# Optimization experiments

Hardware: AMD Instinct MI355X
Metric: run time of the kernel (lower is better)

## Reference

```python
import jax, jax.numpy as jnp
import numpy as np

B, T, NB = 8, 120, 40
VD, WD = 2053, 300
H, E, NH, HD = 512, 256, 8, 64
SEG, NSEG = 12, 10
IDX = np.round(np.linspace(SEG - 1, T - 1, NSEG)).astype(int)  # segment endpoints


def setup_inputs():
    keys = iter(jax.random.split(jax.random.key(0), 64))
    def w(*shape):
        return jax.random.normal(next(keys), shape, jnp.float32) * 0.02
    z = lambda *s: jnp.zeros(s, jnp.float32)
    return dict(
        videos=jax.random.normal(next(keys), (B, T, NB, VD), jnp.float32),
        sub_glove=jax.random.normal(next(keys), (B, WD), jnp.float32),
        obj_glove=jax.random.normal(next(keys), (B, WD), jnp.float32),
        W_ev=w(VD - 5, E), b_ev=z(E),
        W_el=w(5, E), b_el=z(E),
        W_ew=w(WD, E), b_ew=z(E),
        W_sp1=w(2 * E, E), b_sp1=z(E), w_sp2=w(E),
        W_s2o=w(NB, E), b_s2o=z(E),
        W_o2s=w(NB, E), b_o2s=z(E),
        W_tv=w(H, H), b_tv=z(H),
        Wq=w(H, H), bq=z(H), Wk=w(H, H), bk=z(H), Wv=w(H, H), bv=z(H), Wo=w(H, H), bo=z(H),
        g1=jnp.ones(H, jnp.float32), be1=z(H),
        Wf1=w(H, H), bf1=z(H), Wf2=w(H, H), bf2=z(H),
        g2=jnp.ones(H, jnp.float32), be2=z(H),
        W_tr=w(H, H), b_tr=z(H),
        W_tb1=w(2 * H, H), b_tb1=z(H), w_tb2=w(H),
        W_ih=w(4 * H, H), W_hh=w(4 * H, H), b_ih=z(4 * H), b_hh=z(4 * H),
        W_l1=w(2 * H, H), b_l1=z(H), w_l2=w(H),
    )


def reference(videos, sub_glove, obj_glove, W_ev, b_ev, W_el, b_el, W_ew, b_ew,
              W_sp1, b_sp1, w_sp2, W_s2o, b_s2o, W_o2s, b_o2s, W_tv, b_tv,
              Wq, bq, Wk, bk, Wv, bv, Wo, bo, g1, be1, Wf1, bf1, Wf2, bf2, g2, be2,
              W_tr, b_tr, W_tb1, b_tb1, w_tb2, W_ih, W_hh, b_ih, b_hh, W_l1, b_l1, w_l2):
    relu = jax.nn.relu
    # spatialAtt (vectorized over batch; dropout = identity, eval mode)
    ve = relu(videos[..., :VD - 5] @ W_ev + b_ev) + relu(videos[..., VD - 5:] @ W_el + b_el)  # [B,T,NB,E]
    sub_e = relu(sub_glove @ W_ew + b_ew)  # [B,E]
    obj_e = relu(obj_glove @ W_ew + b_ew)

    def attend(word):  # additive attention over bboxes per frame
        wb = jnp.broadcast_to(word[:, None, None, :], ve.shape)
        s = jnp.tanh(jnp.concatenate([ve, wb], -1) @ W_sp1 + b_sp1) @ w_sp2  # [B,T,NB]
        a = jax.nn.softmax(s, -1)
        return jnp.einsum('btn,btne->bte', a, ve), a

    sub_feat, sub_att = attend(sub_e)
    obj_feat, obj_att = attend(obj_e)
    s2o = relu(sub_att @ W_s2o + b_s2o)  # msg_sub2obj on attention weights [B,T,NB]->[B,T,E]
    o2s = relu(obj_att @ W_o2s + b_o2s)
    ori_x = jnp.concatenate([sub_feat + o2s, obj_feat + s2o], -1)  # [B,T,H]
    rel = jnp.concatenate([sub_e, obj_e], -1)[:, None, :]  # [B,1,H]

    def ln(zz, g, b):
        m = zz.mean(-1, keepdims=True)
        v = jnp.mean((zz - m) ** 2, -1, keepdims=True)
        return (zz - m) * jax.lax.rsqrt(v + 1e-5) * g + b

    # transform_visual + 1-layer post-norm TransformerEncoder (relu FFN, dropout=identity)
    x = relu(ori_x @ W_tv + b_tv)
    q = (x @ Wq + bq).reshape(B, T, NH, HD)
    k = (x @ Wk + bk).reshape(B, T, NH, HD)
    v = (x @ Wv + bv).reshape(B, T, NH, HD)
    att = jax.nn.softmax(jnp.einsum('bqhd,bkhd->bhqk', q, k) / np.float32(np.sqrt(HD)), -1)
    ao = jnp.einsum('bhqk,bkhd->bqhd', att, v).reshape(B, T, H) @ Wo + bo
    x = ln(x + ao, g1, be1)
    x = ln(x + relu(x @ Wf1 + bf1) @ Wf2 + bf2, g2, be2)
    within = x  # [B,T,H]

    seg_in = within[:, IDX, :]  # [B,NSEG,H]
    tr = relu(rel @ W_tr + b_tr)
    ctx = jnp.broadcast_to(tr, seg_in.shape)
    beta2 = jax.nn.softmax(jnp.tanh(jnp.concatenate([seg_in, ctx], -1) @ W_tb1 + b_tb1) @ w_tb2, -1)  # [B,NSEG]

    # torch-convention LSTM (gates i,f,g,o); note attention weights are NOT applied to input (vfeat=input)
    def step(carry, xt):
        h, c = carry
        gates = xt @ W_ih.T + h @ W_hh.T + b_ih + b_hh
        i, f, g_, o = jnp.split(gates, 4, -1)
        c = jax.nn.sigmoid(f) * c + jax.nn.sigmoid(i) * jnp.tanh(g_)
        h = jax.nn.sigmoid(o) * jnp.tanh(c)
        return (h, c), h

    (hT, cT), _ = jax.lax.scan(step, (jnp.zeros((B, H), within.dtype), jnp.zeros((B, H), within.dtype)),
                               seg_in.transpose(1, 0, 2))

    ctx2 = jnp.broadcast_to(hT[:, None, :], within.shape)
    beta1 = jax.nn.softmax(jnp.tanh(jnp.concatenate([within, ctx2], -1) @ W_l1 + b_l1) @ w_l2, -1)  # [B,T]
    temp = beta1 + jnp.repeat(beta2, SEG, axis=1)  # temp[:,i] = beta1[:,i] + beta2[:,i//12]
    output = jnp.einsum('bt,bth->bh', temp, within)  # [B,H]
    return output, hT, cT, sub_att, obj_att, beta1, beta2
```

## Files before the change

kernel.cpp:

```cpp
#include <hip/hip_runtime.h>
#include <cstddef>
#include <cstdint>

#define B_ 8
#define T_ 120
#define NB_ 40
#define VD_ 2053
#define E_ 256
#define H_ 512
#define M_ 38400
#define R_ 960

static constexpr size_t OFF_VE    = 0;
static constexpr size_t OFF_SSUB  = OFF_VE + (size_t)M_ * E_;
static constexpr size_t OFF_SOBJ  = OFF_SSUB + M_;
static constexpr size_t OFF_WBS   = OFF_SOBJ + M_;
static constexpr size_t OFF_WBO   = OFF_WBS + B_ * E_;
static constexpr size_t OFF_TBIAS = OFF_WBO + B_ * E_;
static constexpr size_t OFF_ORIX  = OFF_TBIAS + B_ * H_;
static constexpr size_t OFF_X     = OFF_ORIX + (size_t)R_ * H_;
static constexpr size_t OFF_Q     = OFF_X    + (size_t)R_ * H_;
static constexpr size_t OFF_K     = OFF_Q    + (size_t)R_ * H_;
static constexpr size_t OFF_V     = OFF_K    + (size_t)R_ * H_;
static constexpr size_t OFF_AO    = OFF_V    + (size_t)R_ * H_;
static constexpr size_t OFF_ATTN  = OFF_AO   + (size_t)R_ * H_;
static constexpr size_t OFF_X1    = OFF_ATTN + (size_t)R_ * H_;
static constexpr size_t OFF_F1    = OFF_X1   + (size_t)R_ * H_;
static constexpr size_t OFF_F2    = OFF_F1   + (size_t)R_ * H_;
static constexpr size_t OFF_WIN   = OFF_F2   + (size_t)R_ * H_;
static constexpr size_t OFF_WT    = OFF_WIN  + (size_t)R_ * H_;
static constexpr size_t OFF_Z2    = OFF_WT + (size_t)1024 * 2048;
static constexpr size_t OFF_H0    = OFF_Z2 + 128;
static constexpr size_t OFF_HB    = OFF_H0 + 3 * 4096;
static constexpr size_t OFF_L1    = OFF_HB + B_ * H_;
static constexpr size_t OFF_BAR   = OFF_L1 + 960;
static constexpr size_t OFF_END0  = OFF_BAR + 4;
static constexpr size_t OFF_WIH   = (OFF_END0 + 3) & ~(size_t)3;
static constexpr size_t OFF_WHH   = OFF_WIH + 524288;
static constexpr size_t OFF_WL1B  = OFF_WHH + 524288;
static constexpr size_t OFF_WINBF = OFF_WL1B + 131072;
static constexpr size_t OFF_VEBF  = OFF_WINBF + 245760;
static constexpr size_t OFF_END   = OFF_VEBF + (size_t)M_ * E_ / 2;

static constexpr size_t O_OUT  = 0;
static constexpr size_t O_HT   = 4096;
static constexpr size_t O_CT   = 8192;
static constexpr size_t O_SATT = 12288;
static constexpr size_t O_OATT = 50688;
static constexpr size_t O_B1   = 89088;
static constexpr size_t O_B2   = 90048;

#define DEVFN __device__ __forceinline__

typedef __attribute__((ext_vector_type(8))) short short8;
typedef __attribute__((ext_vector_type(4))) float f32x4;

DEVFN float sigf(float x) { return 1.0f / (1.0f + __expf(-x)); }

DEVFN float fast_tanh(float x) {
  float e = __expf(2.f * x);
  return 1.f - 2.f / (e + 1.f);
}

DEVFN unsigned short f2bf(float x) {
  unsigned int u = __float_as_uint(x);
  u += 0x7FFFu + ((u >> 16) & 1u);
  return (unsigned short)(u >> 16);
}
DEVFN float bf2f(unsigned short u) { return __uint_as_float((unsigned int)u << 16); }

DEVFN short8 mk8(const float* f) {
  short8 r;
#pragma unroll
  for (int j = 0; j < 8; ++j) r[j] = (short)f2bf(f[j]);
  return r;
}

DEVFN float wredsum(float v) {
#pragma unroll
  for (int m = 32; m; m >>= 1) v += __shfl_xor(v, m);
  return v;
}
DEVFN float wredmax(float v) {
#pragma unroll
  for (int m = 32; m; m >>= 1) v = fmaxf(v, __shfl_xor(v, m));
  return v;
}

__global__ __launch_bounds__(256) void k_zero(float* p, int n) {
  int i = blockIdx.x * 256 + threadIdx.x;
  if (i < n) p[i] = 0.f;
}

__global__ __launch_bounds__(256) void k_small0(
    const float* __restrict__ sub_g, const float* __restrict__ obj_g,
    const float* __restrict__ W_ew, const float* __restrict__ b_ew,
    const float* __restrict__ W_sp1, const float* __restrict__ b_sp1,
    const float* __restrict__ W_tr, const float* __restrict__ b_tr,
    const float* __restrict__ W_tb1, const float* __restrict__ b_tb1,
    float* __restrict__ wbs, float* __restrict__ wbo, float* __restrict__ tbias) {
  int b = blockIdx.x, tid = threadIdx.x;
  __shared__ float sg[300], og[300], se[256], oe[256], trl[512];
  for (int i = tid; i < 300; i += 256) { sg[i] = sub_g[b * 300 + i]; og[i] = obj_g[b * 300 + i]; }
  __syncthreads();
  {
    float a1 = b_ew[tid], a2 = a1;
    for (int w = 0; w < 300; ++w) {
      float we = W_ew[w * 256 + tid];
      a1 += sg[w] * we; a2 += og[w] * we;
    }
    se[tid] = fmaxf(a1, 0.f); oe[tid] = fmaxf(a2, 0.f);
  }
  __syncthreads();
  {
    float a1 = b_sp1[tid], a2 = a1;
    for (int e = 0; e < 256; ++e) {
      float ww = W_sp1[(256 + e) * 256 + tid];
      a1 += se[e] * ww; a2 += oe[e] * ww;
    }
    wbs[b * 256 + tid] = a1; wbo[b * 256 + tid] = a2;
  }
  for (int jj = 0; jj < 2; ++jj) {
    int j = tid + jj * 256;
    float a = b_tr[j];
    for (int i = 0; i < 256; ++i) a += se[i] * W_tr[i * 512 + j];
    for (int i = 0; i < 256; ++i) a += oe[i] * W_tr[(256 + i) * 512 + j];
    trl[j] = fmaxf(a, 0.f);
  }
  __syncthreads();
  for (int jj = 0; jj < 2; ++jj) {
    int j = tid + jj * 256;
    float a = b_tb1[j];
    for (int i = 0; i < 512; ++i) a += trl[i] * W_tb1[(size_t)(512 + i) * 512 + j];
    tbias[b * 512 + j] = a;
  }
}

__global__ __launch_bounds__(256) void k_wprep(
    const float* __restrict__ W_ev, const float* __restrict__ W_tv,
    const float* __restrict__ Wq, const float* __restrict__ Wk,
    const float* __restrict__ Wv, const float* __restrict__ Wo,
    const float* __restrict__ Wf1, const float* __restrict__ Wf2,
    const float* __restrict__ W_sp1, const float* __restrict__ W_l1,
    const float* __restrict__ W_ih, const float* __restrict__ W_hh,
    const float* __restrict__ sub_g, const float* __restrict__ obj_g,
    const float* __restrict__ W_ew, const float* __restrict__ b_ew,
    const float* __restrict__ b_sp1, const float* __restrict__ W_tr,
    const float* __restrict__ b_tr, const float* __restrict__ W_tb1,
    const float* __restrict__ b_tb1,
    unsigned short* __restrict__ wevbf, unsigned short* __restrict__ w7bf,
    unsigned short* __restrict__ wsp1bf, unsigned short* __restrict__ wl1bf,
    unsigned short* __restrict__ wihbf, unsigned short* __restrict__ whhbf,
    float* __restrict__ hz,
    float* __restrict__ wbs, float* __restrict__ wbo, float* __restrict__ tbias) {
  int bid = blockIdx.x, tid = threadIdx.x;
  __shared__ float shm[64 * 65];
  float (*t)[65] = (float(*)[65])shm;
  if (bid < 128) {
    int kb = bid >> 2, nb = bid & 3;
#pragma unroll
    for (int i = 0; i < 16; ++i) {
      int idx = tid + 256 * i; int r = idx >> 6, c = idx & 63;
      t[r][c] = W_ev[(size_t)(kb * 64 + r) * 256 + nb * 64 + c];
    }
    __syncthreads();
#pragma unroll
    for (int i = 0; i < 16; ++i) {
      int idx = tid + 256 * i; int n = idx >> 6, kk = idx & 63;
      wevbf[(size_t)(nb * 64 + n) * 2048 + kb * 64 + kk] = f2bf(t[kk][n]);
    }
  } else if (bid < 576) {
    int b2 = bid - 128;
    int wsel = b2 >> 6, sub = b2 & 63;
    int kb = sub >> 3, nb = sub & 7;
    const float* src = wsel == 0 ? W_tv : wsel == 1 ? Wq : wsel == 2 ? Wk
                     : wsel == 3 ? Wv : wsel == 4 ? Wo : wsel == 5 ? Wf1 : Wf2;
    unsigned short* dst = w7bf + (size_t)wsel * 262144;
#pragma unroll
    for (int i = 0; i < 16; ++i) {
      int idx = tid + 256 * i; int r = idx >> 6, c = idx & 63;
      t[r][c] = src[(size_t)(kb * 64 + r) * 512 + nb * 64 + c];
    }
    __syncthreads();
#pragma unroll
    for (int i = 0; i < 16; ++i) {
      int idx = tid + 256 * i; int n = idx >> 6, kk = idx & 63;
      dst[(size_t)(nb * 64 + n) * 512 + kb * 64 + kk] = f2bf(t[kk][n]);
    }
  } else if (bid < 592) {
    int b2 = bid - 576;
    int kb = b2 >> 2, nb = b2 & 3;
#pragma unroll
    for (int i = 0; i < 16; ++i) {
      int idx = tid + 256 * i; int r = idx >> 6, c = idx & 63;
      t[r][c] = W_sp1[(size_t)(kb * 64 + r) * 256 + nb * 64 + c];
    }
    __syncthreads();
#pragma unroll
    for (int i = 0; i < 16; ++i) {
      int idx = tid + 256 * i; int n = idx >> 6, kk = idx & 63;
      wsp1bf[(size_t)(nb * 64 + n) * 256 + kb * 64 + kk] = f2bf(t[kk][n]);
    }
  } else if (bid < 656) {
    int b2 = bid - 592;
    int kb = b2 >> 3, nb = b2 & 7;
#pragma unroll
    for (int i = 0; i < 16; ++i) {
      int idx = tid + 256 * i; int r = idx >> 6, c = idx & 63;
      t[r][c] = W_l1[(size_t)(kb * 64 + r) * 512 + nb * 64 + c];
    }
    __syncthreads();
#pragma unroll
    for (int i = 0; i < 16; ++i) {
      int idx = tid + 256 * i; int n = idx >> 6, kk = idx & 63;
      wl1bf[(size_t)(nb * 64 + n) * 512 + kb * 64 + kk] = f2bf(t[kk][n]);
    }
  } else if (bid < 1680) {
    int i = (bid - 656) * 256 + tid;
    const float* s; unsigned short* d; int off;
    if (i < 131072) { s = W_ih; d = wihbf; off = i * 8; }
    else            { s = W_hh; d = whhbf; off = (i - 131072) * 8; }
    float f[8];
#pragma unroll
    for (int j = 0; j < 8; ++j) f[j] = s[off + j];
    *(short8*)(d + off) = mk8(f);
  } else if (bid == 1680) {
    for (int i = tid; i < 12288; i += 256) hz[i] = 0.f;
  } else {
    int b = bid - 1681;
    float* sg = shm;
    float* og = shm + 300;
    float* se = shm + 600;
    float* oe = shm + 856;
    float* trl = shm + 1112;
    for (int i = tid; i < 300; i += 256) { sg[i] = sub_g[b * 300 + i]; og[i] = obj_g[b * 300 + i]; }
    __syncthreads();
    {
      float a1 = b_ew[tid], a2 = a1;
      for (int w = 0; w < 300; ++w) {
        float we = W_ew[w * 256 + tid];
        a1 += sg[w] * we; a2 += og[w] * we;
      }
      se[tid] = fmaxf(a1, 0.f); oe[tid] = fmaxf(a2, 0.f);
    }
    __syncthreads();
    {
      float a1 = b_sp1[tid], a2 = a1;
      for (int e = 0; e < 256; ++e) {
        float ww = W_sp1[(256 + e) * 256 + tid];
        a1 += se[e] * ww; a2 += oe[e] * ww;
      }
      wbs[b * 256 + tid] = a1; wbo[b * 256 + tid] = a2;
    }
    for (int jj = 0; jj < 2; ++jj) {
      int j = tid + jj * 256;
      float a = b_tr[j];
      for (int i = 0; i < 256; ++i) a += se[i] * W_tr[i * 512 + j];
      for (int i = 0; i < 256; ++i) a += oe[i] * W_tr[(256 + i) * 512 + j];
      trl[j] = fmaxf(a, 0.f);
    }
    __syncthreads();
    for (int jj = 0; jj < 2; ++jj) {
      int j = tid + jj * 256;
      float a = b_tb1[j];
      for (int i = 0; i < 512; ++i) a += trl[i] * W_tb1[(size_t)(512 + i) * 512 + j];
      tbias[b * 512 + j] = a;
    }
  }
}

__global__ __launch_bounds__(256) void k_wconvT(const float* __restrict__ src,
                                                unsigned short* __restrict__ dst,
                                                int K, int N) {
  __shared__ float t[64][65];
  int nblk = N >> 6;
  int kb = blockIdx.x / nblk, nb = blockIdx.x - kb * nblk;
  int tid = threadIdx.x;
#pragma unroll
  for (int i = 0; i < 16; ++i) {
    int idx = tid + 256 * i;
    int r = idx >> 6, c = idx & 63;
    t[r][c] = src[(size_t)(kb * 64 + r) * N + nb * 64 + c];
  }
  __syncthreads();
#pragma unroll
  for (int i = 0; i < 16; ++i) {
    int idx = tid + 256 * i;
    int n = idx >> 6, kk = idx & 63;
    dst[(size_t)(nb * 64 + n) * K + kb * 64 + kk] = f2bf(t[kk][n]);
  }
}

__global__ __launch_bounds__(256) void k_wconv7(
    const float* __restrict__ w0, const float* __restrict__ w1,
    const float* __restrict__ w2, const float* __restrict__ w3,
    const float* __restrict__ w4, const float* __restrict__ w5,
    const float* __restrict__ w6, unsigned short* __restrict__ dstb) {
  __shared__ float t[64][65];
  int wsel = blockIdx.x >> 6, sub = blockIdx.x & 63;
  int kb = sub >> 3, nb = sub & 7;
  const float* src = wsel == 0 ? w0 : wsel == 1 ? w1 : wsel == 2 ? w2
                   : wsel == 3 ? w3 : wsel == 4 ? w4 : wsel == 5 ? w5 : w6;
  unsigned short* dst = dstb + (size_t)wsel * 262144;
  int tid = threadIdx.x;
#pragma unroll
  for (int i = 0; i < 16; ++i) {
    int idx = tid + 256 * i;
    int r = idx >> 6, c = idx & 63;
    t[r][c] = src[(size_t)(kb * 64 + r) * 512 + nb * 64 + c];
  }
  __syncthreads();
#pragma unroll
  for (int i = 0; i < 16; ++i) {
    int idx = tid + 256 * i;
    int n = idx >> 6, kk = idx & 63;
    dst[(size_t)(nb * 64 + n) * 512 + kb * 64 + kk] = f2bf(t[kk][n]);
  }
}

__global__ __launch_bounds__(256) void k_cvt2(const float* __restrict__ a,
                                              const float* __restrict__ b,
                                              unsigned short* __restrict__ da,
                                              unsigned short* __restrict__ db) {
  int i = blockIdx.x * 256 + threadIdx.x;
  const float* s; unsigned short* d; int off;
  if (i < 131072) { s = a; d = da; off = i * 8; }
  else            { s = b; d = db; off = (i - 131072) * 8; }
  float f[8];
#pragma unroll
  for (int j = 0; j < 8; ++j) f[j] = s[off + j];
  *(short8*)(d + off) = mk8(f);
}

#define VESTEP(FA, KA, KB)                                                 \
  {                                                                        \
    short8 ha = mk8(FA);                                                   \
    __syncthreads();                                                       \
    *(short8*)(lds + dstA) = ha;                                           \
    _Pragma("unroll")                                                      \
    for (int i = 0; i < 4; ++i) *(short8*)(lds + dstB[i]) = stB[i];        \
    __syncthreads();                                                       \
    _Pragma("unroll")                                                      \
    for (int j = 0; j < 8; ++j) FA[j] = apA[(KA) + j];                     \
    _Pragma("unroll")                                                      \
    for (int i = 0; i < 4; ++i) stB[i] = *(const short8*)(spB[i] + (KB));  \
    _Pragma("unroll")                                                      \
    for (int kk = 0; kk < 2; ++kk) {                                       \
      short8 a8[4], b8[2];                                                 \
      _Pragma("unroll")                                                    \
      for (int fm = 0; fm < 4; ++fm) {                                     \
        int row = fm * 16 + l16;                                           \
        a8[fm] = *(const short8*)(lds + row * 64 +                         \
                                  (((kk * 4 + lk) ^ (row & 7)) * 8));      \
      }                                                                    \
      _Pragma("unroll")                                                    \
      for (int fn = 0; fn < 2; ++fn) {                                     \
        int n = wid * 32 + fn * 16 + l16;                                  \
        b8[fn] = *(const short8*)(lds + 4096 + n * 64 +                    \
                                  (((kk * 4 + lk) ^ (n & 7)) * 8));        \
      }                                                                    \
      _Pragma("unroll")                                                    \
      for (int fm = 0; fm < 4; ++fm)                                       \
        _Pragma("unroll")                                                  \
        for (int fn = 0; fn < 2; ++fn)                                     \
          acc[fm][fn] = __builtin_amdgcn_mfma_f32_16x16x32_bf16(           \
              a8[fm], b8[fn], acc[fm][fn], 0, 0, 0);                       \
    }                                                                      \
  }

__global__ __launch_bounds__(512) void k_gemm_ve_m97(
    const float* __restrict__ videos, const unsigned short* __restrict__ wtbf,
    const float* __restrict__ bev, const float* __restrict__ Wel,
    const float* __restrict__ bel, unsigned short* __restrict__ vebf) {
  __shared__ __align__(16) unsigned short lds[20480];
  int tid = threadIdx.x;
  int rowbase = blockIdx.x * 64;
  int lane = tid & 63, wid = tid >> 6;
  int l16 = lane & 15, lk = lane >> 4;

  int arow = tid >> 3, akc = tid & 7;
  const float* apA = videos + (size_t)(rowbase + arow) * VD_ + akc * 8;
  int dstA = arow * 64 + ((akc ^ (arow & 7)) * 8);
  const unsigned short* spB[4];
  int dstB[4];
#pragma unroll
  for (int i = 0; i < 4; ++i) {
    int g = tid + 512 * i;
    int n = g >> 3, kc = g & 7;
    spB[i] = wtbf + (size_t)n * 2048 + kc * 8;
    dstB[i] = 4096 + n * 64 + ((kc ^ (n & 7)) * 8);
  }
  float fa0[8], fa1[8];
  short8 stB[4];
#pragma unroll
  for (int j = 0; j < 8; ++j) fa0[j] = apA[j];
#pragma unroll
  for (int i = 0; i < 4; ++i) stB[i] = *(const short8*)(spB[i]);
#pragma unroll
  for (int j = 0; j < 8; ++j) fa1[j] = apA[64 + j];

  f32x4 acc[4][2] = {};
  for (int k0 = 0; k0 < 2048; k0 += 128) {
    int ka0 = k0 + 128; if (ka0 >= 2048) ka0 -= 2048;
    int kb0 = k0 + 64;
    VESTEP(fa0, ka0, kb0);
    int ka1 = k0 + 192; if (ka1 >= 2048) ka1 -= 2048;
    int kb1 = k0 + 128; if (kb1 >= 2048) kb1 -= 2048;
    VESTEP(fa1, ka1, kb1);
  }
  float bevv[2], belv[2], w5[5][2];
#pragma unroll
  for (int fn = 0; fn < 2; ++fn) {
    int col = wid * 32 + fn * 16 + l16;
    bevv[fn] = bev[col]; belv[fn] = bel[col];
#pragma unroll
    for (int kk = 0; kk < 5; ++kk) w5[kk][fn] = Wel[kk * 256 + col];
  }
#pragma unroll
  for (int fm = 0; fm < 4; ++fm) {
#pragma unroll
    for (int r = 0; r < 4; ++r) {
      int grow = rowbase + fm * 16 + lk * 4 + r;
      const float* vt = videos + (size_t)grow * VD_ + 2048;
      float t0 = vt[0], t1 = vt[1], t2 = vt[2], t3 = vt[3], t4 = vt[4];
      unsigned short* vob = vebf + (size_t)grow * 256;
#pragma unroll
      for (int fn = 0; fn < 2; ++fn) {
        int col = wid * 32 + fn * 16 + l16;
        float s2 = belv[fn] + t0 * w5[0][fn] + t1 * w5[1][fn] + t2 * w5[2][fn] +
                   t3 * w5[3][fn] + t4 * w5[4][fn];
        float vvv = fmaxf(acc[fm][fn][r] + bevv[fn], 0.f) + fmaxf(s2, 0.f);
        vob[col] = f2bf(vvv);
      }
    }
  }
}

__global__ __launch_bounds__(256) void k_score_bf(
    const unsigned short* __restrict__ vebf, const unsigned short* __restrict__ wsp1,
    const float* __restrict__ w_sp2, const float* __restrict__ wbs,
    const float* __restrict__ wbo, float* __restrict__ s_sub,
    float* __restrict__ s_obj) {
  __shared__ float reds[4][64], redo_[4][64];
  int tid = threadIdx.x;
  int rowbase = blockIdx.x * 64;
  int lane = tid & 63, wid = tid >> 6;
  int l16 = lane & 15, lk = lane >> 4;
  const unsigned short* ap[4];
  const unsigned short* bp[4];
#pragma unroll
  for (int fm = 0; fm < 4; ++fm)
    ap[fm] = vebf + (size_t)(rowbase + fm * 16 + l16) * 256 + lk * 8;
#pragma unroll
  for (int fn = 0; fn < 4; ++fn)
    bp[fn] = wsp1 + (size_t)(wid * 64 + fn * 16 + l16) * 256 + lk * 8;
  f32x4 acc[4][4] = {};
#pragma unroll 2
  for (int k0 = 0; k0 < 256; k0 += 32) {
    short8 a8[4], b8[4];
#pragma unroll
    for (int fm = 0; fm < 4; ++fm) a8[fm] = *(const short8*)(ap[fm] + k0);
#pragma unroll
    for (int fn = 0; fn < 4; ++fn) b8[fn] = *(const short8*)(bp[fn] + k0);
#pragma unroll
    for (int fm = 0; fm < 4; ++fm)
#pragma unroll
      for (int fn = 0; fn < 4; ++fn)
        acc[fm][fn] = __builtin_amdgcn_mfma_f32_16x16x32_bf16(
            a8[fm], b8[fn], acc[fm][fn], 0, 0, 0);
  }
  int b = rowbase / 4800;
  float w2[4], bs[4], bo[4];
#pragma unroll
  for (int fn = 0; fn < 4; ++fn) {
    int col = wid * 64 + fn * 16 + l16;
    w2[fn] = w_sp2[col];
    bs[fn] = wbs[b * 256 + col];
    bo[fn] = wbo[b * 256 + col];
  }
  float ps[4][4], po[4][4];
#pragma unroll
  for (int fm = 0; fm < 4; ++fm)
#pragma unroll
    for (int r = 0; r < 4; ++r) {
      float aps = 0, apo = 0;
#pragma unroll
      for (int fn = 0; fn < 4; ++fn) {
        float t = acc[fm][fn][r];
        aps += fast_tanh(t + bs[fn]) * w2[fn];
        apo += fast_tanh(t + bo[fn]) * w2[fn];
      }
      ps[fm][r] = aps;
      po[fm][r] = apo;
    }
#pragma unroll
  for (int m = 1; m < 16; m <<= 1) {
#pragma unroll
    for (int fm = 0; fm < 4; ++fm)
#pragma unroll
      for (int r = 0; r < 4; ++r) {
        ps[fm][r] += __shfl_xor(ps[fm][r], m);
        po[fm][r] += __shfl_xor(po[fm][r], m);
      }
  }
  if (l16 == 0) {
#pragma unroll
    for (int fm = 0; fm < 4; ++fm)
#pragma unroll
      for (int r = 0; r < 4; ++r) {
        int row = fm * 16 + lk * 4 + r;
        reds[wid][row] = ps[fm][r];
        redo_[wid][row] = po[fm][r];
      }
  }
  __syncthreads();
  if (tid < 64) {
    float s1 = reds[0][tid] + reds[1][tid] + reds[2][tid] + reds[3][tid];
    float s2 = redo_[0][tid] + redo_[1][tid] + redo_[2][tid] + redo_[3][tid];
    s_sub[rowbase + tid] = s1;
    s_obj[rowbase + tid] = s2;
  }
}

__global__ __launch_bounds__(256) void k_attend_bf(
    const float* __restrict__ s_sub, const float* __restrict__ s_obj,
    const unsigned short* __restrict__ vebf, const float* __restrict__ W_s2o,
    const float* __restrict__ b_s2o, const float* __restrict__ W_o2s,
    const float* __restrict__ b_o2s, float* __restrict__ out_satt,
    float* __restrict__ out_oatt, float* __restrict__ orix) {
  int row = blockIdx.x;
  int tid = threadIdx.x;
  __shared__ float alds[2][40];
  int wv = tid >> 6, lane = tid & 63;
  if (wv < 2) {
    const float* sarr = (wv ? s_obj : s_sub) + row * 40;
    float v = (lane < 40) ? sarr[lane] : -1e30f;
    float mx = wredmax(v);
    float e = (lane < 40) ? __expf(v - mx) : 0.f;
    float sm = wredsum(e);
    float p = e / sm;
    if (lane < 40) {
      alds[wv][lane] = p;
      (wv ? out_oatt : out_satt)[row * 40 + lane] = p;
    }
  }
  __syncthreads();
  int e = tid;
  const unsigned short* vrow = vebf + (size_t)row * 40 * 256;
  float sf = 0, of = 0, s2o = b_s2o[e], o2s = b_o2s[e];
  for (int n = 0; n < 40; ++n) {
    float as = alds[0][n], aob = alds[1][n];
    float vv = bf2f(vrow[n * 256 + e]);
    sf += as * vv;
    of += aob * vv;
    s2o += as * W_s2o[n * 256 + e];
    o2s += aob * W_o2s[n * 256 + e];
  }
  s2o = fmaxf(s2o, 0.f);
  o2s = fmaxf(o2s, 0.f);
  orix[(size_t)row * 512 + e] = sf + o2s;
  orix[(size_t)row * 512 + 256 + e] = of + s2o;
}

__global__ __launch_bounds__(256) void k_gemm_ve_mfma(
    const float* __restrict__ videos, const unsigned short* __restrict__ wtbf,
    const float* __restrict__ bev, const float* __restrict__ Wel,
    const float* __restrict__ bel, float* __restrict__ ve) {
  int tid = threadIdx.x;
  int rowbase = blockIdx.x * 64;
  int lane = tid & 63, wid = tid >> 6;
  int l16 = lane & 15, lk = lane >> 4;
  const float* ap[4];
  const unsigned short* bp[4];
#pragma unroll
  for (int fm = 0; fm < 4; ++fm)
    ap[fm] = videos + (size_t)(rowbase + fm * 16 + l16) * VD_ + lk * 8;
#pragma unroll
  for (int fn = 0; fn < 4; ++fn)
    bp[fn] = wtbf + (size_t)(wid * 64 + fn * 16 + l16) * 2048 + lk * 8;
  f32x4 acc[4][4] = {};
  for (int k0 = 0; k0 < 2048; k0 += 64) {
#pragma unroll
    for (int kk = 0; kk < 2; ++kk) {
      int ko = k0 + kk * 32;
      short8 a8[4], b8[4];
#pragma unroll
      for (int fm = 0; fm < 4; ++fm) {
        const float* a = ap[fm] + ko;
        float f[8];
#pragma unroll
        for (int j = 0; j < 8; ++j) f[j] = a[j];
        a8[fm] = mk8(f);
      }
#pragma unroll
      for (int fn = 0; fn < 4; ++fn) b8[fn] = *(const short8*)(bp[fn] + ko);
#pragma unroll
      for (int fm = 0; fm < 4; ++fm)
#pragma unroll
        for (int fn = 0; fn < 4; ++fn)
          acc[fm][fn] = __builtin_amdgcn_mfma_f32_16x16x32_bf16(
              a8[fm], b8[fn], acc[fm][fn], 0, 0, 0);
    }
    if ((k0 & 255) == 192) __builtin_amdgcn_s_barrier();
  }
  float bevv[4], belv[4], w5[5][4];
#pragma unroll
  for (int fn = 0; fn < 4; ++fn) {
    int col = wid * 64 + fn * 16 + l16;
    bevv[fn] = bev[col]; belv[fn] = bel[col];
#pragma unroll
    for (int kk = 0; kk < 5; ++kk) w5[kk][fn] = Wel[kk * 256 + col];
  }
#pragma unroll
  for (int fm = 0; fm < 4; ++fm) {
#pragma unroll
    for (int r = 0; r < 4; ++r) {
      int grow = rowbase + fm * 16 + lk * 4 + r;
      const float* vt = videos + (size_t)grow * VD_ + 2048;
      float t0 = vt[0], t1 = vt[1], t2 = vt[2], t3 = vt[3], t4 = vt[4];
      float* vo = ve + (size_t)grow * 256;
#pragma unroll
      for (int fn = 0; fn < 4; ++fn) {
        int col = wid * 64 + fn * 16 + l16;
        float s2 = belv[fn] + t0 * w5[0][fn] + t1 * w5[1][fn] + t2 * w5[2][fn] +
                   t3 * w5[3][fn] + t4 * w5[4][fn];
        vo[col] = fmaxf(acc[fm][fn][r] + bevv[fn], 0.f) + fmaxf(s2, 0.f);
      }
    }
  }
}

__global__ __launch_bounds__(256) void k_score(
    const float* __restrict__ ve, const float* __restrict__ W_sp1,
    const float* __restrict__ w_sp2, const float* __restrict__ wbs,
    const float* __restrict__ wbo, float* __restrict__ s_sub,
    float* __restrict__ s_obj) {
  __shared__ float vel[32][264];
  int tid = threadIdx.x;
  int rowbase = blockIdx.x * 32;
  for (int i = tid; i < 2048; i += 256) {
    int r = i >> 6, c = (i & 63) << 2;
    *(float4*)&vel[r][c] = *(const float4*)&ve[(size_t)(rowbase + r) * 256 + c];
  }
  __syncthreads();
  int wv = tid >> 6, lane = tid & 63;
  int r0 = wv * 8;
  float acc[8][4] = {};
  for (int k = 0; k < 256; ++k) {
    float w4[4];
#pragma unroll
    for (int c = 0; c < 4; ++c) w4[c] = W_sp1[(size_t)k * 256 + c * 64 + lane];
#pragma unroll
    for (int m = 0; m < 8; ++m) {
      float a = vel[r0 + m][k];
#pragma unroll
      for (int c = 0; c < 4; ++c) acc[m][c] += a * w4[c];
    }
  }
  int b = rowbase / 4800;
  float w2[4], bs[4], bo[4];
#pragma unroll
  for (int c = 0; c < 4; ++c) {
    int col = c * 64 + lane;
    w2[c] = w_sp2[col];
    bs[c] = wbs[b * 256 + col];
    bo[c] = wbo[b * 256 + col];
  }
#pragma unroll
  for (int m = 0; m < 8; ++m) {
    float ps = 0, po = 0;
#pragma unroll
    for (int c = 0; c < 4; ++c) {
      float t = acc[m][c];
      ps += fast_tanh(t + bs[c]) * w2[c];
      po += fast_tanh(t + bo[c]) * w2[c];
    }
    ps = wredsum(ps);
    po = wredsum(po);
    if (lane == 0) {
      s_sub[rowbase + r0 + m] = ps;
      s_obj[rowbase + r0 + m] = po;
    }
  }
}

__global__ __launch_bounds__(256) void k_attend(
    const float* __restrict__ s_sub, const float* __restrict__ s_obj,
    const float* __restrict__ ve, const float* __restrict__ W_s2o,
    const float* __restrict__ b_s2o, const float* __restrict__ W_o2s,
    const float* __restrict__ b_o2s, float* __restrict__ out_satt,
    float* __restrict__ out_oatt, float* __restrict__ orix) {
  int row = blockIdx.x;
  int tid = threadIdx.x;
  __shared__ float alds[2][40];
  int wv = tid >> 6, lane = tid & 63;
  if (wv < 2) {
    const float* sarr = (wv ? s_obj : s_sub) + row * 40;
    float v = (lane < 40) ? sarr[lane] : -1e30f;
    float mx = wredmax(v);
    float e = (lane < 40) ? __expf(v - mx) : 0.f;
    float sm = wredsum(e);
    float p = e / sm;
    if (lane < 40) {
      alds[wv][lane] = p;
      (wv ? out_oatt : out_satt)[row * 40 + lane] = p;
    }
  }
  __syncthreads();
  int e = tid;
  const float* vrow = ve + (size_t)row * 40 * 256;
  float sf = 0, of = 0, s2o = b_s2o[e], o2s = b_o2s[e];
  for (int n = 0; n < 40; ++n) {
    float as = alds[0][n], aob = alds[1][n];
    float vv = vrow[n * 256 + e];
// ... 501 lines not shown
}

__global__ __launch_bounds__(256) void k_final(
    const float* __restrict__ l1, const float* __restrict__ z2,
    const float* __restrict__ within, const float* __restrict__ hT,
    const float* __restrict__ cT, float* __restrict__ dout) {
  int b = blockIdx.x;
  int tid = threadIdx.x;
  __shared__ float temp[120];
  __shared__ float b2[10];
  int wv = tid >> 6, lane = tid & 63;
  if (wv == 1) {
    float v = (lane < 10) ? z2[b * 10 + lane] : -1e30f;
    float mx = wredmax(v);
    float e = (lane < 10) ? __expf(v - mx) : 0.f;
    float sm = wredsum(e);
    if (lane < 10) {
      float p = e / sm;
      b2[lane] = p;
      dout[O_B2 + b * 10 + lane] = p;
    }
  }
  if (wv == 0) {
    float v1 = l1[b * 120 + lane];
    float v2 = (lane + 64 < 120) ? l1[b * 120 + 64 + lane] : -1e30f;
    float mx = wredmax(fmaxf(v1, v2));
    float e1 = __expf(v1 - mx);
    float e2 = (lane + 64 < 120) ? __expf(v2 - mx) : 0.f;
    float sm = wredsum(e1 + e2);
    float p1 = e1 / sm;
    dout[O_B1 + b * 120 + lane] = p1;
    temp[lane] = p1;
    if (lane + 64 < 120) {
      float p2 = e2 / sm;
      dout[O_B1 + b * 120 + 64 + lane] = p2;
      temp[64 + lane] = p2;
    }
  }
  __syncthreads();
  for (int t = tid; t < 120; t += 256) temp[t] += b2[t / 12];
  __syncthreads();
  for (int hh = tid; hh < 512; hh += 256) {
    float o = 0;
    for (int t = 0; t < 120; ++t) o += temp[t] * within[(size_t)(b * 120 + t) * 512 + hh];
    dout[O_OUT + b * 512 + hh] = o;
    dout[O_HT + b * 512 + hh] = hT[b * 512 + hh];
    dout[O_CT + b * 512 + hh] = cT[b * 512 + hh];
  }
}

extern "C" void kernel_launch(void* const* d_in, const int* in_sizes, int n_in,
                              void* d_out, int out_size, void* d_ws, size_t ws_size,
                              hipStream_t stream) {
  const float* videos = (const float*)d_in[0];
  const float* sub_g  = (const float*)d_in[1];
  const float* obj_g  = (const float*)d_in[2];
  const float* W_ev   = (const float*)d_in[3];
  const float* b_ev   = (const float*)d_in[4];
  const float* W_el   = (const float*)d_in[5];
  const float* b_el   = (const float*)d_in[6];
  const float* W_ew   = (const float*)d_in[7];
  const float* b_ew   = (const float*)d_in[8];
  const float* W_sp1  = (const float*)d_in[9];
  const float* b_sp1  = (const float*)d_in[10];
  const float* w_sp2  = (const float*)d_in[11];
  const float* W_s2o  = (const float*)d_in[12];
  const float* b_s2o  = (const float*)d_in[13];
  const float* W_o2s  = (const float*)d_in[14];
  const float* b_o2s  = (const float*)d_in[15];
  const float* W_tv   = (const float*)d_in[16];
  const float* b_tv   = (const float*)d_in[17];
  const float* Wq     = (const float*)d_in[18];
  const float* bq     = (const float*)d_in[19];
  const float* Wk     = (const float*)d_in[20];
  const float* bk     = (const float*)d_in[21];
  const float* Wv     = (const float*)d_in[22];
  const float* bv     = (const float*)d_in[23];
  const float* Wo     = (const float*)d_in[24];
  const float* bo     = (const float*)d_in[25];
  const float* g1     = (const float*)d_in[26];
  const float* be1    = (const float*)d_in[27];
  const float* Wf1    = (const float*)d_in[28];
  const float* bf1    = (const float*)d_in[29];
  const float* Wf2    = (const float*)d_in[30];
  const float* bf2    = (const float*)d_in[31];
  const float* g2     = (const float*)d_in[32];
  const float* be2    = (const float*)d_in[33];
  const float* W_tr   = (const float*)d_in[34];
  const float* b_tr   = (const float*)d_in[35];
  const float* W_tb1  = (const float*)d_in[36];
  const float* b_tb1  = (const float*)d_in[37];
  const float* w_tb2  = (const float*)d_in[38];
  const float* W_ih   = (const float*)d_in[39];
  const float* W_hh   = (const float*)d_in[40];
  const float* b_ih   = (const float*)d_in[41];
  const float* b_hh   = (const float*)d_in[42];
  const float* W_l1   = (const float*)d_in[43];
  const float* b_l1   = (const float*)d_in[44];
  const float* w_l2   = (const float*)d_in[45];

  float* out = (float*)d_out;
  float* w = (float*)d_ws;

  float* ve_p   = w + OFF_VE;
  float* ssub_p = w + OFF_SSUB;
  float* sobj_p = w + OFF_SOBJ;
  float* wbs_p  = w + OFF_WBS;
  float* wbo_p  = w + OFF_WBO;
  float* tb_p   = w + OFF_TBIAS;
  float* orix_p = w + OFF_ORIX;
  float* x_p    = w + OFF_X;
  float* q_p    = w + OFF_Q;
  float* k_p    = w + OFF_K;
  float* v_p    = w + OFF_V;
  float* ao_p   = w + OFF_AO;
  float* attn_p = w + OFF_ATTN;
  float* x1_p   = w + OFF_X1;
  float* f1_p   = w + OFF_F1;
  float* f2_p   = w + OFF_F2;
  float* win_p  = w + OFF_WIN;
  float* z2_p   = w + OFF_Z2;
  float* h_p    = w + OFF_H0;
  float* c_p    = h_p + 2 * 4096;
  float* hb_p   = w + OFF_HB;
  float* l1_p   = w + OFF_L1;

  unsigned short* wtbase = (unsigned short*)(w + OFF_WT);
  unsigned short* wevbf = wtbase;
  unsigned short* w7bf  = wtbase + 524288;
  unsigned short* wtvbf = w7bf;
  unsigned short* wqbf  = w7bf + 1 * 262144;
  unsigned short* wobf  = w7bf + 4 * 262144;
  unsigned short* wf1bf = w7bf + 5 * 262144;
  unsigned short* wf2bf = w7bf + 6 * 262144;
  unsigned short* wsp1bf = w7bf + 7 * 262144;
  unsigned short* wihbf  = (unsigned short*)(w + OFF_WIH);
  unsigned short* whhbf  = (unsigned short*)(w + OFF_WHH);
  unsigned short* wl1bf  = (unsigned short*)(w + OFF_WL1B);
  unsigned short* winbf_p = (unsigned short*)(w + OFF_WINBF);
  unsigned short* vebf_p = (unsigned short*)(w + OFF_VEBF);
  float* gx_p = w + OFF_Q;
  const bool big = ws_size >= (size_t)OFF_END * 4;

  if (big) {
    k_wprep<<<1689, 256, 0, stream>>>(W_ev, W_tv, Wq, Wk, Wv, Wo, Wf1, Wf2,
                                      W_sp1, W_l1, W_ih, W_hh, sub_g, obj_g,
                                      W_ew, b_ew, b_sp1, W_tr, b_tr, W_tb1,
                                      b_tb1, wevbf, w7bf, wsp1bf, wl1bf, wihbf,
                                      whhbf, h_p, wbs_p, wbo_p, tb_p);
    k_gemm_ve_m97<<<600, 512, 0, stream>>>(videos, wevbf, b_ev, W_el, b_el,
                                           vebf_p);
    k_score_bf<<<600, 256, 0, stream>>>(vebf_p, wsp1bf, w_sp2, wbs_p, wbo_p,
                                        ssub_p, sobj_p);
    k_attend_bf<<<960, 256, 0, stream>>>(ssub_p, sobj_p, vebf_p, W_s2o, b_s2o,
                                         W_o2s, b_o2s, out + O_SATT,
                                         out + O_OATT, orix_p);
    k_gemm_h<<<240, 256, 0, stream>>>(orix_p, wtvbf, b_tv, b_tv, b_tv, x_p, 8, 1);
    k_gemm_h<<<720, 256, 0, stream>>>(x_p, wqbf, bq, bk, bv, q_p, 24, 0);
    k_mha<<<256, 256, 0, stream>>>(q_p, k_p, v_p, ao_p);
    k_gemm_h<<<240, 256, 0, stream>>>(ao_p, wobf, bo, bo, bo, attn_p, 8, 0);
    k_ln<<<240, 256, 0, stream>>>(x_p, attn_p, g1, be1, x1_p, nullptr);
    k_gemm_h<<<240, 256, 0, stream>>>(x1_p, wf1bf, bf1, bf1, bf1, f1_p, 8, 1);
    k_gemm_h<<<240, 256, 0, stream>>>(f1_p, wf2bf, bf2, bf2, bf2, f2_p, 8, 0);
    k_ln<<<240, 256, 0, stream>>>(x1_p, f2_p, g2, be2, win_p, winbf_p);
    k_xb<<<144, 256, 0, stream>>>(win_p, wihbf, b_ih, b_hh, gx_p, W_tb1, w_tb2,
                                  tb_p, z2_p);
    for (int s = 0; s < 10; ++s) {
      float* hin = h_p + (s & 1) * 4096;
      float* hout = h_p + ((s & 1) ^ 1) * 4096;
      k_lstm_step<<<32, 128, 0, stream>>>(hin, whhbf, gx_p, s, hout, c_p);
    }
    k_hbias<<<16, 256, 0, stream>>>(h_p, W_l1, b_l1, hb_p);
    k_beta1_bf<<<15, 256, 0, stream>>>(winbf_p, wl1bf, w_l2, hb_p, l1_p);
    k_final<<<8, 256, 0, stream>>>(l1_p, z2_p, win_p, h_p, c_p, out);
  } else {
    unsigned short* wihbf_a = (unsigned short*)(w + OFF_Q + 163840);
    unsigned short* whhbf_a = (unsigned short*)(w + OFF_Q + 688128);
    k_zero<<<48, 256, 0, stream>>>(h_p, 3 * 4096);
    k_small0<<<8, 256, 0, stream>>>(sub_g, obj_g, W_ew, b_ew, W_sp1, b_sp1,
                                    W_tr, b_tr, W_tb1, b_tb1, wbs_p, wbo_p, tb_p);
    k_wconvT<<<128, 256, 0, stream>>>(W_ev, wevbf, 2048, 256);
    k_wconv7<<<448, 256, 0, stream>>>(W_tv, Wq, Wk, Wv, Wo, Wf1, Wf2, w7bf);
    k_gemm_ve_mfma<<<600, 256, 0, stream>>>(videos, wevbf, b_ev, W_el, b_el, ve_p);
    k_score<<<1200, 256, 0, stream>>>(ve_p, W_sp1, w_sp2, wbs_p, wbo_p, ssub_p, sobj_p);
    k_attend<<<960, 256, 0, stream>>>(ssub_p, sobj_p, ve_p, W_s2o, b_s2o, W_o2s,
                                      b_o2s, out + O_SATT, out + O_OATT, orix_p);
    k_gemm_h<<<240, 256, 0, stream>>>(orix_p, wtvbf, b_tv, b_tv, b_tv, x_p, 8, 1);
    k_gemm_h<<<720, 256, 0, stream>>>(x_p, wqbf, bq, bk, bv, q_p, 24, 0);
    k_mha<<<256, 256, 0, stream>>>(q_p, k_p, v_p, ao_p);
    k_gemm_h<<<240, 256, 0, stream>>>(ao_p, wobf, bo, bo, bo, attn_p, 8, 0);
    k_ln<<<240, 256, 0, stream>>>(x_p, attn_p, g1, be1, x1_p, nullptr);
    k_gemm_h<<<240, 256, 0, stream>>>(x1_p, wf1bf, bf1, bf1, bf1, f1_p, 8, 1);
    k_gemm_h<<<240, 256, 0, stream>>>(f1_p, wf2bf, bf2, bf2, bf2, f2_p, 8, 0);
    k_ln<<<240, 256, 0, stream>>>(x1_p, f2_p, g2, be2, win_p, nullptr);
    k_cvt2<<<1024, 256, 0, stream>>>(W_ih, W_hh, wihbf_a, whhbf_a);
    k_xproj<<<64, 256, 0, stream>>>(win_p, wihbf_a, b_ih, b_hh, gx_p);
    k_beta2<<<80, 256, 0, stream>>>(win_p, W_tb1, w_tb2, tb_p, z2_p);
    for (int s = 0; s < 10; ++s) {
      float* hin = h_p + (s & 1) * 4096;
      float* hout = h_p + ((s & 1) ^ 1) * 4096;
      k_lstm_step<<<32, 128, 0, stream>>>(hin, whhbf_a, gx_p, s, hout, c_p);
    }
    k_hbias<<<16, 256, 0, stream>>>(h_p, W_l1, b_l1, hb_p);
    k_beta1<<<240, 256, 0, stream>>>(win_p, W_l1, w_l2, hb_p, l1_p);
    k_final<<<8, 256, 0, stream>>>(l1_p, z2_p, win_p, h_p, c_p, out);
  }
}
```

Measured before the change: 631.0 us.

## Double-buffer LDS in video GEMM and vectorize attend kernel per-wave rows

The main video-embedding GEMM moves from a single LDS buffer with two barriers per k-step to a ping-pong double buffer. The next tile's global loads are issued before the MFMA compute, and only one barrier is needed per step, so load latency overlaps compute. The cost is double the LDS footprint, which may lower occupancy. Separately, the attend kernel now processes four rows per block, one wave each, using 4-wide vector loads and stores instead of one row per block with scalar accesses.

Measured after the change: 638.3 us. No clear change (+1.2%).

```diff
diff --git a/kernel.cpp b/kernel.cpp
--- a/kernel.cpp
+++ b/kernel.cpp
@@ -53,6 +53,7 @@
 #define DEVFN __device__ __forceinline__
 
 typedef __attribute__((ext_vector_type(8))) short short8;
+typedef __attribute__((ext_vector_type(4))) short short4v;
 typedef __attribute__((ext_vector_type(4))) float f32x4;
 
 DEVFN float sigf(float x) { return 1.0f / (1.0f + __expf(-x)); }
@@ -332,47 +333,55 @@
   *(short8*)(d + off) = mk8(f);
 }
 
-#define VESTEP(FA, KA, KB)                                                 \
-  {                                                                        \
-    short8 ha = mk8(FA);                                                   \
-    __syncthreads();                                                       \
-    *(short8*)(lds + dstA) = ha;                                           \
-    _Pragma("unroll")                                                      \
-    for (int i = 0; i < 4; ++i) *(short8*)(lds + dstB[i]) = stB[i];        \
-    __syncthreads();                                                       \
-    _Pragma("unroll")                                                      \
-    for (int j = 0; j < 8; ++j) FA[j] = apA[(KA) + j];                     \
-    _Pragma("unroll")                                                      \
-    for (int i = 0; i < 4; ++i) stB[i] = *(const short8*)(spB[i] + (KB));  \
-    _Pragma("unroll")                                                      \
-    for (int kk = 0; kk < 2; ++kk) {                                       \
-      short8 a8[4], b8[2];                                                 \
-      _Pragma("unroll")                                                    \
-      for (int fm = 0; fm < 4; ++fm) {                                     \
-        int row = fm * 16 + l16;                                           \
-        a8[fm] = *(const short8*)(lds + row * 64 +                         \
-                                  (((kk * 4 + lk) ^ (row & 7)) * 8));      \
-      }                                                                    \
-      _Pragma("unroll")                                                    \
-      for (int fn = 0; fn < 2; ++fn) {                                     \
-        int n = wid * 32 + fn * 16 + l16;                                  \
-        b8[fn] = *(const short8*)(lds + 4096 + n * 64 +                    \
-                                  (((kk * 4 + lk) ^ (n & 7)) * 8));        \
-      }                                                                    \
-      _Pragma("unroll")                                                    \
-      for (int fm = 0; fm < 4; ++fm)                                       \
-        _Pragma("unroll")                                                  \
-        for (int fn = 0; fn < 2; ++fn)                                     \
-          acc[fm][fn] = __builtin_amdgcn_mfma_f32_16x16x32_bf16(           \
-              a8[fm], b8[fn], acc[fm][fn], 0, 0, 0);                       \
-    }                                                                      \
+#define VECOMPUTE(RDBASE)                                                   \
+  _Pragma("unroll")                                                         \
+  for (int kk = 0; kk < 2; ++kk) {                                          \
+    short8 a8[4], b8[2];                                                    \
+    _Pragma("unroll")                                                       \
+    for (int fm = 0; fm < 4; ++fm) {                                        \
+      int row = fm * 16 + l16;                                              \
+      a8[fm] = *(const short8*)(lds + (RDBASE) + row * 64 +                 \
+                                (((kk * 4 + lk) ^ (row & 7)) * 8));         \
+    }                                                                       \
+    _Pragma("unroll")                                                       \
+    for (int fn = 0; fn < 2; ++fn) {                                        \
+      int n = wid * 32 + fn * 16 + l16;                                     \
+      b8[fn] = *(const short8*)(lds + (RDBASE) + 4096 + n * 64 +            \
+                                (((kk * 4 + lk) ^ (n & 7)) * 8));           \
+    }                                                                       \
+    _Pragma("unroll")                                                       \
+    for (int fm = 0; fm < 4; ++fm)                                          \
+      _Pragma("unroll")                                                     \
+      for (int fn = 0; fn < 2; ++fn)                                        \
+        acc[fm][fn] = __builtin_amdgcn_mfma_f32_16x16x32_bf16(              \
+            a8[fm], b8[fn], acc[fm][fn], 0, 0, 0);                          \
+  }
+
+#define VESTEP(RDBASE, WRBASE, KNEXT)                                       \
+  {                                                                         \
+    bool pre = (KNEXT) < 2048;                                              \
+    if (pre) {                                                              \
+      _Pragma("unroll")                                                     \
+      for (int j = 0; j < 8; ++j) fa[j] = apA[(KNEXT) + j];                 \
+      _Pragma("unroll")                                                     \
+      for (int i = 0; i < 4; ++i) stB[i] = *(const short8*)(spB[i] + (KNEXT)); \
+    }                                                                       \
+    VECOMPUTE(RDBASE);                                                      \
+    if (pre) {                                                              \
+      short8 ha = mk8(fa);                                                  \
+      *(short8*)(lds + (WRBASE) + dstA) = ha;                               \
+      _Pragma("unroll")                                                     \
+      for (int i = 0; i < 4; ++i)                                           \
+        *(short8*)(lds + (WRBASE) + dstB[i]) = stB[i];                      \
+      __syncthreads();                                                      \
+    }                                                                       \
   }
 
 __global__ __launch_bounds__(512) void k_gemm_ve_m97(
     const float* __restrict__ videos, const unsigned short* __restrict__ wtbf,
     const float* __restrict__ bev, const float* __restrict__ Wel,
     const float* __restrict__ bel, unsigned short* __restrict__ vebf) {
-  __shared__ __align__(16) unsigned short lds[20480];
+  __shared__ __align__(16) unsigned short lds[40960];
   int tid = threadIdx.x;
   int rowbase = blockIdx.x * 64;
   int lane = tid & 63, wid = tid >> 6;
@@ -390,23 +399,24 @@
     spB[i] = wtbf + (size_t)n * 2048 + kc * 8;
     dstB[i] = 4096 + n * 64 + ((kc ^ (n & 7)) * 8);
   }
-  float fa0[8], fa1[8];
+  float fa[8];
   short8 stB[4];
 #pragma unroll
-  for (int j = 0; j < 8; ++j) fa0[j] = apA[j];
+  for (int j = 0; j < 8; ++j) fa[j] = apA[j];
 #pragma unroll
   for (int i = 0; i < 4; ++i) stB[i] = *(const short8*)(spB[i]);
-#pragma unroll
-  for (int j = 0; j < 8; ++j) fa1[j] = apA[64 + j];
+  {
+    short8 ha = mk8(fa);
+    *(short8*)(lds + dstA) = ha;
+#pragma unroll
+    for (int i = 0; i < 4; ++i) *(short8*)(lds + dstB[i]) = stB[i];
+  }
+  __syncthreads();
 
   f32x4 acc[4][2] = {};
   for (int k0 = 0; k0 < 2048; k0 += 128) {
-    int ka0 = k0 + 128; if (ka0 >= 2048) ka0 -= 2048;
-    int kb0 = k0 + 64;
-    VESTEP(fa0, ka0, kb0);
-    int ka1 = k0 + 192; if (ka1 >= 2048) ka1 -= 2048;
-    int kb1 = k0 + 128; if (kb1 >= 2048) kb1 -= 2048;
-    VESTEP(fa1, ka1, kb1);
+    VESTEP(0, 20480, k0 + 64);
+    VESTEP(20480, 0, k0 + 128);
   }
   float bevv[2], belv[2], w5[5][2];
 #pragma unroll
@@ -528,38 +538,60 @@
     const float* __restrict__ b_s2o, const float* __restrict__ W_o2s,
     const float* __restrict__ b_o2s, float* __restrict__ out_satt,
     float* __restrict__ out_oatt, float* __restrict__ orix) {
-  int row = blockIdx.x;
-  int tid = threadIdx.x;
-  __shared__ float alds[2][40];
+  __shared__ float alds[4][2][40];
+  int tid = threadIdx.x;
   int wv = tid >> 6, lane = tid & 63;
-  if (wv < 2) {
-    const float* sarr = (wv ? s_obj : s_sub) + row * 40;
+  int row = blockIdx.x * 4 + wv;
+  {
+    const float* sarr = s_sub + row * 40;
     float v = (lane < 40) ? sarr[lane] : -1e30f;
     float mx = wredmax(v);
     float e = (lane < 40) ? __expf(v - mx) : 0.f;
     float sm = wredsum(e);
-    float p = e / sm;
     if (lane < 40) {
-      alds[wv][lane] = p;
-      (wv ? out_oatt : out_satt)[row * 40 + lane] = p;
-    }
-  }
-  __syncthreads();
-  int e = tid;
-  const unsigned short* vrow = vebf + (size_t)row * 40 * 256;
-  float sf = 0, of = 0, s2o = b_s2o[e], o2s = b_o2s[e];
+      float p = e / sm;
+      alds[wv][0][lane] = p;
+      out_satt[row * 40 + lane] = p;
+    }
+    sarr = s_obj + row * 40;
+    v = (lane < 40) ? sarr[lane] : -1e30f;
+    mx = wredmax(v);
+    e = (lane < 40) ? __expf(v - mx) : 0.f;
+    sm = wredsum(e);
+    if (lane < 40) {
+      float p = e / sm;
+      alds[wv][1][lane] = p;
+      out_oatt[row * 40 + lane] = p;
+    }
+  }
+  __syncthreads();
+  int e0 = lane * 4;
+  const unsigned short* vrow = vebf + (size_t)row * 40 * 256 + e0;
+  f32x4 sf = {}, of = {}, s2o, o2s;
+#pragma unroll
+  for (int c = 0; c < 4; ++c) { s2o[c] = b_s2o[e0 + c]; o2s[c] = b_o2s[e0 + c]; }
   for (int n = 0; n < 40; ++n) {
-    float as = alds[0][n], aob = alds[1][n];
-    float vv = bf2f(vrow[n * 256 + e]);
-    sf += as * vv;
-    of += aob * vv;
-    s2o += as * W_s2o[n * 256 + e];
-    o2s += aob * W_o2s[n * 256 + e];
-  }
-  s2o = fmaxf(s2o, 0.f);
-  o2s = fmaxf(o2s, 0.f);
-  orix[(size_t)row * 512 + e] = sf + o2s;
-  orix[(size_t)row * 512 + 256 + e] = of + s2o;
+    float as = alds[wv][0][n], aob = alds[wv][1][n];
+    short4v v4 = *(const short4v*)(vrow + n * 256);
+    f32x4 ws = *(const f32x4*)(W_s2o + n * 256 + e0);
+    f32x4 wo = *(const f32x4*)(W_o2s + n * 256 + e0);
+#pragma unroll
+    for (int c = 0; c < 4; ++c) {
+      float vv = bf2f((unsigned short)v4[c]);
+      sf[c] += as * vv;
+      of[c] += aob * vv;
+      s2o[c] += as * ws[c];
+      o2s[c] += aob * wo[c];
+    }
+  }
+  f32x4 r1, r2;
+#pragma unroll
+  for (int c = 0; c < 4; ++c) {
+    r1[c] = sf[c] + fmaxf(o2s[c], 0.f);
+    r2[c] = of[c] + fmaxf(s2o[c], 0.f);
+  }
+  *(f32x4*)(orix + (size_t)row * 512 + e0) = r1;
+  *(f32x4*)(orix + (size_t)row * 512 + 256 + e0) = r2;
 }
 
 __global__ __launch_bounds__(256) void k_gemm_ve_mfma(
@@ -1367,7 +1399,7 @@
                                            vebf_p);
     k_score_bf<<<600, 256, 0, stream>>>(vebf_p, wsp1bf, w_sp2, wbs_p, wbo_p,
                                         ssub_p, sobj_p);
-    k_attend_bf<<<960, 256, 0, stream>>>(ssub_p, sobj_p, vebf_p, W_s2o, b_s2o,
+    k_attend_bf<<<240, 256, 0, stream>>>(ssub_p, sobj_p, vebf_p, W_s2o, b_s2o,
                                          W_o2s, b_o2s, out + O_SATT,
                                          out + O_OATT, orix_p);
     k_gemm_h<<<240, 256, 0, stream>>>(orix_p, wtvbf, b_tv, b_tv, b_tv, x_p, 8, 1);
```
